# Kernel optimization log

Measured on AMD Instinct MI355X. Metric: run time of the kernel, lower is better.

Reference implementation:

```python
import jax, jax.numpy as jnp
import numpy as np

EPS = 1e-6  # clamp epsilon in GeM
NORM_EPS = 1e-12  # torch F.normalize eps
PATCH_SIZES = (3,)


def l2norm(x, axis):
    n = jnp.sqrt(jnp.sum(x * x, axis=axis, keepdims=True))
    return x / jnp.maximum(n, NORM_EPS)


def setup_inputs() -> dict:
    key = jax.random.key(0)
    k1, k2, k3 = jax.random.split(key, 3)
    N, D, H, W, F = 16, 2048, 32, 32, 512
    x = jax.random.normal(k1, (N, D, H, W), jnp.float32)
    proj_w = jax.random.normal(k2, (F, D), jnp.float32) * (1.0 / np.sqrt(D))
    proj_b = jax.random.normal(k3, (F,), jnp.float32) * 0.01
    p = jnp.full((1,), 3.0, jnp.float32)
    return {"x": x, "proj_w": proj_w, "proj_b": proj_b, "p": p}


def reference(x, proj_w, proj_b, p):
    # ---- GeM global descriptor (global_pool path inside local_pool) ----
    x = l2norm(x, axis=1)                                  # L2 over channel dim
    g = jnp.clip(x, EPS, None) ** p[0]                     # [N,D,H,W]
    g = g.mean(axis=(-2, -1))                              # [N,D]
    g = g ** (1.0 / p[0])
    g = g @ proj_w.T + proj_b                              # [N,F]
    g = l2norm(g, axis=1)

    # ---- integral image over spatial dims ----
    integ = jnp.cumsum(jnp.cumsum(x, axis=-1), axis=-2)    # [N,D,H,W]

    local_descs = []
    for ps in PATCH_SIZES:
        off = ps // 2
        # zero-pad (1+off) on top/left, then replicate-pad off on bottom/right
        ipad = jnp.pad(integ, ((0, 0), (0, 0), (1 + off, 0), (1 + off, 0)))
        ipad = jnp.pad(ipad, ((0, 0), (0, 0), (0, off), (0, off)), mode='edge')
        # box sum via 4-corner integral-image difference
        # == grouped 2x2 conv with dilation=ps, weights [[1,-1],[-1,1]], stride=1
        box = (ipad[:, :, :-ps, :-ps] - ipad[:, :, :-ps, ps:]
               - ipad[:, :, ps:, :-ps] + ipad[:, :, ps:, ps:])  # [N,D,H,W]
        N, D, Hh, Ww = box.shape
        pd = box.reshape(N, D, Hh * Ww).transpose(0, 2, 1)  # [N,HW,D]
        pd = pd @ proj_w.T + proj_b                         # [N,HW,F]
        pd = l2norm(pd, axis=2)
        local_descs.append(pd.transpose(0, 2, 1))           # [N,F,HW]

    return g, local_descs[0]
```

## Files before the change

### kernel.cpp

```cpp
#include <hip/hip_runtime.h>
#include <hip/hip_bf16.h>

#define N_ 16
#define D_ 2048
#define H_ 32
#define W_ 32
#define HW_ 1024
#define F_ 512

typedef unsigned short u16;
typedef unsigned int u32;
typedef __attribute__((ext_vector_type(8))) short bf16x8;
typedef __attribute__((ext_vector_type(4))) float f32x4;

__device__ __forceinline__ u16 f2bf(float f) {
  union { float fv; u32 u; } c; c.fv = f;
  u32 u = c.u;
  u32 r = (u + 0x7fffu + ((u >> 16) & 1u)) >> 16;
  return (u16)r;
}

#define GLD_LDS16(gp, lp) __builtin_amdgcn_global_load_lds( \
    (const __attribute__((address_space(1))) void*)(gp), \
    (__attribute__((address_space(3))) void*)(lp), 16, 0, 0)

__global__ __launch_bounds__(256) void k_zero(float* __restrict__ p) {
  int i = blockIdx.x * 256 + threadIdx.x;
  ((float4*)p)[i] = (float4){0.f, 0.f, 0.f, 0.f};
}

__global__ __launch_bounds__(256) void k_sumsq(const float* __restrict__ x, float* __restrict__ sumsq) {
  const int n = blockIdx.x;
  const int dc = blockIdx.y;
  const int t = threadIdx.x;
  const float* xp = x + ((size_t)n * D_ + (size_t)dc * 64) * HW_;
  float s0 = 0.f, s1 = 0.f, s2 = 0.f, s3 = 0.f;
  for (int d = 0; d < 64; ++d) {
    const float* row = xp + (size_t)d * HW_;
    float v0 = row[t], v1 = row[t + 256], v2 = row[t + 512], v3 = row[t + 768];
    s0 += v0 * v0; s1 += v1 * v1; s2 += v2 * v2; s3 += v3 * v3;
  }
  atomicAdd(&sumsq[n * HW_ + t      ], s0);
  atomicAdd(&sumsq[n * HW_ + t + 256], s1);
  atomicAdd(&sumsq[n * HW_ + t + 512], s2);
  atomicAdd(&sumsq[n * HW_ + t + 768], s3);
}

__global__ __launch_bounds__(256) void k_box2(const float* __restrict__ x,
    const float* __restrict__ sumsq, const float* __restrict__ pvec,
    float* __restrict__ gbuf, u16* __restrict__ packA) {
  const int n = blockIdx.x, ht = blockIdx.y, dc = blockIdx.z;
  const int h0 = ht * 4, d0 = dc * 64;
  const int t = threadIdx.x;
  const int w = t & 31, g = t >> 5;
  const float p = pvec[0];
  const bool p3 = (p == 3.0f);

  __shared__ __align__(16) u16 sbox[128 * 68];

  float rn[6];
  #pragma unroll
  for (int jj = 0; jj < 6; ++jj) {
    int hp = h0 - 1 + jj;
    float r = 0.f;
    if (hp >= 0 && hp < H_) r = 1.0f / fmaxf(sqrtf(sumsq[n * HW_ + hp * W_ + w]), 1e-12f);
    rn[jj] = r;
  }

  float s[8];
  #pragma unroll
  for (int j = 0; j < 8; ++j) s[j] = 0.f;

  #pragma unroll 2
  for (int j = 0; j < 8; ++j) {
    const int d = d0 + g * 8 + j;
    const float* col = x + ((size_t)(n * D_ + d)) * HW_ + w;
    float v[6];
    #pragma unroll
    for (int jj = 0; jj < 6; ++jj) {
      int hp = h0 - 1 + jj;
      float xv = (hp >= 0 && hp < H_) ? col[hp * W_] : 0.f;
      v[jj] = xv * rn[jj];
    }
    #pragma unroll
    for (int jj = 1; jj <= 4; ++jj) {
      float cv = fmaxf(v[jj], 1e-6f);
      s[j] += p3 ? cv * cv * cv : __powf(cv, p);
    }
    float hs[6];
    #pragma unroll
    for (int jj = 0; jj < 6; ++jj) {
      float l = __shfl_up(v[jj], 1, 32);
      float r = __shfl_down(v[jj], 1, 32);
      if (w == 0) l = 0.f;
      if (w == 31) r = 0.f;
      hs[jj] = l + v[jj] + r;
    }
    #pragma unroll
    for (int k = 0; k < 4; ++k) {
      float b = hs[k] + hs[k + 1] + hs[k + 2];
      sbox[(k * 32 + w) * 68 + g * 8 + j] = f2bf(b);
    }
  }
  __syncthreads();

  {
    const int r = t >> 1, half = t & 1;
    const u16* srcp = sbox + r * 68 + half * 32;
    uint2 a[8];
    #pragma unroll
    for (int q = 0; q < 8; ++q) a[q] = *(const uint2*)(srcp + q * 4);
    const int mt = n * 16 + ht * 2 + (r >> 6);
    const int mf = (r >> 4) & 3, r15 = r & 15;
    const int kt = dc * 2 + half;
    u16* dst = packA + ((size_t)(mt * 64 + kt) * 4 + mf) * 512 + r15 * 8;
    #pragma unroll
    for (int q = 0; q < 4; ++q) {
      uint4 b;
      b.x = a[2 * q].x; b.y = a[2 * q].y; b.z = a[2 * q + 1].x; b.w = a[2 * q + 1].y;
      *(uint4*)(dst + q * 128) = b;
    }
  }

  #pragma unroll
  for (int j = 0; j < 8; ++j) {
    float v = s[j];
    v += __shfl_xor(v, 16, 32);
    v += __shfl_xor(v, 8, 32);
    v += __shfl_xor(v, 4, 32);
    v += __shfl_xor(v, 2, 32);
    v += __shfl_xor(v, 1, 32);
    if (w == 0) atomicAdd(&gbuf[n * D_ + d0 + g * 8 + j], v);
  }
}

__global__ __launch_bounds__(256) void k_wconv(const float* __restrict__ w, u16* __restrict__ packB) {
  const int i = blockIdx.x * 256 + threadIdx.x;
  const int lane = i & 63, nf = (i >> 6) & 3, kt = (i >> 8) & 63, wq = i >> 14;
  const int r15 = lane & 15, hi = lane >> 4;
  const int f = wq * 64 + nf * 16 + r15;
  const int k = kt * 32 + hi * 8;
  const float* src = w + (size_t)f * D_ + k;
  float4 v0 = *(const float4*)(src);
  float4 v1 = *(const float4*)(src + 4);
  u16 r[8] = { f2bf(v0.x), f2bf(v0.y), f2bf(v0.z), f2bf(v0.w),
               f2bf(v1.x), f2bf(v1.y), f2bf(v1.z), f2bf(v1.w) };
  *(uint4*)(packB + (size_t)i * 8) = *(const uint4*)r;
}

__global__ __launch_bounds__(512) void k_gemm(const u16* __restrict__ packA,
    const u16* __restrict__ packB, const float* __restrict__ bias,
    float* __restrict__ outL) {
  const int n  = blockIdx.x >> 4;
  const int mtl = blockIdx.x & 15;
  const int mt = blockIdx.x;
  const int hw0 = mtl * 64;
  const int t = threadIdx.x;
  const int lane = t & 63, wv = t >> 6;
  const int r15 = lane & 15, hi = lane >> 4;

  __shared__ __align__(16) float smem_f[128 * 68];
  __shared__ float s_sq[8][64];
  __shared__ float s_rn[64];

  f32x4 acc[4][4];
  #pragma unroll
  for (int a = 0; a < 4; ++a)
    #pragma unroll
    for (int b = 0; b < 4; ++b) acc[a][b] = (f32x4){0.f, 0.f, 0.f, 0.f};

  const u16* asrc = packA + ((size_t)(mt * 64) * 4 + (wv & 3)) * 512 + lane * 8;
  const u16* bbase = packB + (size_t)wv * 131072 + lane * 8;

#define STAGE_A(KT) GLD_LDS16(asrc + (size_t)(KT) * 2048, \
    (char*)smem_f + ((KT) & 7) * 4096 + (wv & 3) * 1024)

  bf16x8 bc[4], bn[4];
  #pragma unroll
  for (int nf = 0; nf < 4; ++nf) bc[nf] = *(const bf16x8*)(bbase + nf * 512);
  __builtin_amdgcn_sched_barrier(0);
  #pragma unroll
  for (int q = 0; q < 5; ++q) STAGE_A(q);
  __builtin_amdgcn_sched_barrier(0);

  for (int kt = 0; kt < 64; ++kt) {
    if (kt + 1 < 64) {
      #pragma unroll
      for (int nf = 0; nf < 4; ++nf)
        bn[nf] = *(const bf16x8*)(bbase + ((kt + 1) * 4 + nf) * 512);
    }
    __builtin_amdgcn_sched_barrier(0);
    if (kt == 0) {
      asm volatile("s_waitcnt vmcnt(9)" ::: "memory");
    } else if (kt < 60) {
      asm volatile("s_waitcnt vmcnt(5)" ::: "memory");
    } else if (kt < 63) {
      asm volatile("s_waitcnt vmcnt(4)" ::: "memory");
    } else {
      asm volatile("s_waitcnt vmcnt(0)" ::: "memory");
    }
    __builtin_amdgcn_sched_barrier(0);
    __builtin_amdgcn_s_barrier();
    __builtin_amdgcn_sched_barrier(0);
    if (kt <= 58) STAGE_A(kt + 5);
    __builtin_amdgcn_sched_barrier(0);

    const u16* sA = (const u16*)((const char*)smem_f + (kt & 7) * 4096);
    bf16x8 af[4];
    #pragma unroll
    for (int mf = 0; mf < 4; ++mf)
      af[mf] = *(const bf16x8*)(sA + mf * 512 + lane * 8);
    #pragma unroll
    for (int mf = 0; mf < 4; ++mf)
      #pragma unroll
      for (int nf = 0; nf < 4; ++nf)
        acc[mf][nf] = __builtin_amdgcn_mfma_f32_16x16x32_bf16(af[mf], bc[nf], acc[mf][nf], 0, 0, 0);
    #pragma unroll
    for (int nf = 0; nf < 4; ++nf) bc[nf] = bn[nf];
  }
#undef STAGE_A

  float badd[4];
  #pragma unroll
  for (int nf = 0; nf < 4; ++nf) badd[nf] = bias[wv * 64 + nf * 16 + r15];
  #pragma unroll
  for (int mf = 0; mf < 4; ++mf)
    #pragma unroll
    for (int nf = 0; nf < 4; ++nf)
      #pragma unroll
      for (int j = 0; j < 4; ++j) acc[mf][nf][j] += badd[nf];

  #pragma unroll
  for (int mf = 0; mf < 4; ++mf)
    #pragma unroll
    for (int j = 0; j < 4; ++j) {
      float s = 0.f;
      #pragma unroll
      for (int nf = 0; nf < 4; ++nf) { float v = acc[mf][nf][j]; s += v * v; }
      s += __shfl_xor(s, 1); s += __shfl_xor(s, 2); s += __shfl_xor(s, 4); s += __shfl_xor(s, 8);
      if ((lane & 15) == 0) s_sq[wv][mf * 16 + hi * 4 + j] = s;
    }
  __syncthreads();
  if (t < 64) {
    float s = 0.f;
    #pragma unroll
    for (int w8 = 0; w8 < 8; ++w8) s += s_sq[w8][t];
    s_rn[t] = 1.0f / fmaxf(sqrtf(s), 1e-12f);
  }
  __syncthreads();

  float* ct = smem_f;
  for (int nf = 0; nf < 4; ++nf) {
    const int fi = wv * 16 + r15;
    #pragma unroll
    for (int mf = 0; mf < 4; ++mf)
      #pragma unroll
      for (int j = 0; j < 4; ++j) {
        int m = mf * 16 + hi * 4 + j;
        ct[fi * 68 + m] = acc[mf][nf][j] * s_rn[m];
      }
    __syncthreads();
    {
      int fr = t >> 2, mq = t & 3;
      int f = (fr >> 4) * 64 + nf * 16 + (fr & 15);
      float* dst = outL + ((size_t)(n * F_ + f)) * HW_ + hw0 + mq * 16;
      const float* srcp = ct + fr * 68 + mq * 16;
      float4 a0 = *(const float4*)(srcp);
      float4 a1 = *(const float4*)(srcp + 4);
      float4 a2 = *(const float4*)(srcp + 8);
      float4 a3 = *(const float4*)(srcp + 12);
      *(float4*)(dst) = a0; *(float4*)(dst + 4) = a1;
      *(float4*)(dst + 8) = a2; *(float4*)(dst + 12) = a3;
    }
    __syncthreads();
  }
}

__global__ __launch_bounds__(256) void k_gem_fin(const float* __restrict__ gbuf,
    const float* __restrict__ pvec, float* __restrict__ gg) {
  int i = blockIdx.x * 256 + threadIdx.x;
  float p = pvec[0];
  float m = gbuf[i] * (1.0f / 1024.0f);
  gg[i] = (p == 3.0f) ? cbrtf(m) : powf(m, 1.0f / p);
}

__global__ __launch_bounds__(256) void k_gproj(const float* __restrict__ w,
    const float* __restrict__ bias, const float* __restrict__ gg,
    float* __restrict__ gproj) {
  const int f = blockIdx.x;
  const int t = threadIdx.x;
  float wreg[8];
  #pragma unroll
  for (int j = 0; j < 8; ++j) wreg[j] = w[(size_t)f * D_ + t + j * 256];
  __shared__ float red[4];
  const int lane = t & 63, wv = t >> 6;
  for (int n = 0; n < N_; ++n) {
    float s = 0.f;
    #pragma unroll
    for (int j = 0; j < 8; ++j) s += wreg[j] * gg[n * D_ + t + j * 256];
    #pragma unroll
    for (int off = 32; off >= 1; off >>= 1) s += __shfl_down(s, off);
    if (lane == 0) red[wv] = s;
    __syncthreads();
    if (t == 0) gproj[n * F_ + f] = red[0] + red[1] + red[2] + red[3] + bias[f];
    __syncthreads();
  }
}

__global__ __launch_bounds__(512) void k_gnorm(const float* __restrict__ gproj, float* __restrict__ outg) {
  const int n = blockIdx.x;
  const int t = threadIdx.x;
  float v = gproj[n * F_ + t];
  float s = v * v;
  const int lane = t & 63, wv = t >> 6;
  #pragma unroll
  for (int off = 32; off >= 1; off >>= 1) s += __shfl_down(s, off);
  __shared__ float red[8];
  __shared__ float rtot;
  if (lane == 0) red[wv] = s;
  __syncthreads();
  if (t == 0) {
    float a = 0.f;
    #pragma unroll
    for (int i = 0; i < 8; ++i) a += red[i];
    rtot = 1.0f / fmaxf(sqrtf(a), 1e-12f);
  }
  __syncthreads();
  outg[n * F_ + t] = v * rtot;
}

extern "C" void kernel_launch(void* const* d_in, const int* in_sizes, int n_in,
                              void* d_out, int out_size, void* d_ws, size_t ws_size,
                              hipStream_t stream) {
  const float* x  = (const float*)d_in[0];
  const float* pw = (const float*)d_in[1];
  const float* pb = (const float*)d_in[2];
  const float* pv = (const float*)d_in[3];
  float* out = (float*)d_out;

  char* ws = (char*)d_ws;
  float* sumsq = (float*)ws;
  float* gbuf  = (float*)(ws + 65536);
  float* gg    = (float*)(ws + 65536 + 131072);
  float* gproj = (float*)(ws + 65536 + 2 * 131072);
  u16*   packB = (u16*)(ws + 65536 + 2 * 131072 + 32768);
  u16*   packA = (u16*)(ws + 4u * 1024u * 1024u);

  k_zero<<<dim3(48), dim3(256), 0, stream>>>(sumsq);
  k_sumsq<<<dim3(16, 32), dim3(256), 0, stream>>>(x, sumsq);
  k_wconv<<<dim3(512), dim3(256), 0, stream>>>(pw, packB);
  k_box2<<<dim3(16, 8, 32), dim3(256), 0, stream>>>(x, sumsq, pv, gbuf, packA);
  k_gem_fin<<<dim3(128), dim3(256), 0, stream>>>(gbuf, pv, gg);
  k_gproj<<<dim3(512), dim3(256), 0, stream>>>(pw, pb, gg, gproj);
  k_gnorm<<<dim3(16), dim3(512), 0, stream>>>(gproj, out);
  k_gemm<<<dim3(256), dim3(512), 0, stream>>>(packA, packB, pb, out + N_ * F_);
}
```

Baseline: 153.7 us.

## Stream box filter over rows per block and deepen B-prefetch in GEMM

```diff
diff --git a/kernel.cpp b/kernel.cpp
--- a/kernel.cpp
+++ b/kernel.cpp
@@ -49,8 +49,8 @@
 __global__ __launch_bounds__(256) void k_box2(const float* __restrict__ x,
     const float* __restrict__ sumsq, const float* __restrict__ pvec,
     float* __restrict__ gbuf, u16* __restrict__ packA) {
-  const int n = blockIdx.x, ht = blockIdx.y, dc = blockIdx.z;
-  const int h0 = ht * 4, d0 = dc * 64;
+  const int n = blockIdx.x, dc = blockIdx.y;
+  const int d0 = dc * 64;
   const int t = threadIdx.x;
   const int w = t & 31, g = t >> 5;
   const float p = pvec[0];
@@ -58,68 +58,77 @@
 
   __shared__ __align__(16) u16 sbox[128 * 68];
 
-  float rn[6];
-  #pragma unroll
-  for (int jj = 0; jj < 6; ++jj) {
-    int hp = h0 - 1 + jj;
-    float r = 0.f;
-    if (hp >= 0 && hp < H_) r = 1.0f / fmaxf(sqrtf(sumsq[n * HW_ + hp * W_ + w]), 1e-12f);
-    rn[jj] = r;
-  }
-
-  float s[8];
-  #pragma unroll
-  for (int j = 0; j < 8; ++j) s[j] = 0.f;
-
-  #pragma unroll 2
-  for (int j = 0; j < 8; ++j) {
-    const int d = d0 + g * 8 + j;
-    const float* col = x + ((size_t)(n * D_ + d)) * HW_ + w;
-    float v[6];
-    #pragma unroll
-    for (int jj = 0; jj < 6; ++jj) {
-      int hp = h0 - 1 + jj;
-      float xv = (hp >= 0 && hp < H_) ? col[hp * W_] : 0.f;
-      v[jj] = xv * rn[jj];
-    }
-    #pragma unroll
-    for (int jj = 1; jj <= 4; ++jj) {
-      float cv = fmaxf(v[jj], 1e-6f);
-      s[j] += p3 ? cv * cv * cv : __powf(cv, p);
-    }
-    float hs[6];
-    #pragma unroll
-    for (int jj = 0; jj < 6; ++jj) {
-      float l = __shfl_up(v[jj], 1, 32);
-      float r = __shfl_down(v[jj], 1, 32);
+  const float* xb = x + ((size_t)(n * D_ + d0 + g * 8)) * HW_ + w;
+  const float* sq = sumsq + n * HW_ + w;
+
+  float hc0[8], hc1[8], s[8];
+  {
+    float rn0 = 1.0f / fmaxf(sqrtf(sq[0]), 1e-12f);
+    #pragma unroll
+    for (int j = 0; j < 8; ++j) {
+      float v = xb[(size_t)j * HW_] * rn0;
+      float cv = fmaxf(v, 1e-6f);
+      s[j] = p3 ? cv * cv * cv : __powf(cv, p);
+      float l = __shfl_up(v, 1, 32), r = __shfl_down(v, 1, 32);
       if (w == 0) l = 0.f;
       if (w == 31) r = 0.f;
-      hs[jj] = l + v[jj] + r;
-    }
-    #pragma unroll
-    for (int k = 0; k < 4; ++k) {
-      float b = hs[k] + hs[k + 1] + hs[k + 2];
-      sbox[(k * 32 + w) * 68 + g * 8 + j] = f2bf(b);
-    }
-  }
-  __syncthreads();
-
-  {
-    const int r = t >> 1, half = t & 1;
-    const u16* srcp = sbox + r * 68 + half * 32;
-    uint2 a[8];
-    #pragma unroll
-    for (int q = 0; q < 8; ++q) a[q] = *(const uint2*)(srcp + q * 4);
-    const int mt = n * 16 + ht * 2 + (r >> 6);
-    const int mf = (r >> 4) & 3, r15 = r & 15;
-    const int kt = dc * 2 + half;
-    u16* dst = packA + ((size_t)(mt * 64 + kt) * 4 + mf) * 512 + r15 * 8;
+      hc0[j] = 0.f;
+      hc1[j] = l + v + r;
+    }
+  }
+
+  for (int ht = 0; ht < 8; ++ht) {
+    const int h0 = ht * 4;
+    float rnr[4];
     #pragma unroll
     for (int q = 0; q < 4; ++q) {
-      uint4 b;
-      b.x = a[2 * q].x; b.y = a[2 * q].y; b.z = a[2 * q + 1].x; b.w = a[2 * q + 1].y;
-      *(uint4*)(dst + q * 128) = b;
-    }
+      int hp = h0 + 1 + q;
+      rnr[q] = (hp < H_) ? 1.0f / fmaxf(sqrtf(sq[hp * W_]), 1e-12f) : 0.f;
+    }
+    #pragma unroll
+    for (int j = 0; j < 8; ++j) {
+      float hsq[4];
+      #pragma unroll
+      for (int q = 0; q < 4; ++q) {
+        int hp = h0 + 1 + q;
+        float v = 0.f;
+        if (hp < H_) {
+          v = xb[(size_t)j * HW_ + hp * W_] * rnr[q];
+          float cv = fmaxf(v, 1e-6f);
+          s[j] += p3 ? cv * cv * cv : __powf(cv, p);
+        }
+        float l = __shfl_up(v, 1, 32), r = __shfl_down(v, 1, 32);
+        if (w == 0) l = 0.f;
+        if (w == 31) r = 0.f;
+        hsq[q] = l + v + r;
+      }
+      u16* sb = sbox + (g * 8 + j);
+      sb[(0 * 32 + w) * 68] = f2bf(hc0[j] + hc1[j] + hsq[0]);
+      sb[(1 * 32 + w) * 68] = f2bf(hc1[j] + hsq[0] + hsq[1]);
+      sb[(2 * 32 + w) * 68] = f2bf(hsq[0] + hsq[1] + hsq[2]);
+      sb[(3 * 32 + w) * 68] = f2bf(hsq[1] + hsq[2] + hsq[3]);
+      hc0[j] = hsq[2];
+      hc1[j] = hsq[3];
+    }
+    __syncthreads();
+    {
+      const int r = t >> 1, half = t & 1;
+      const u16* srcp = sbox + r * 68 + half * 32;
+      uint2 a[8];
+      #pragma unroll
+      for (int q = 0; q < 8; ++q) a[q] = *(const uint2*)(srcp + q * 4);
+      const int mt = n * 16 + ht * 2 + (r >> 6);
+      const int mf = (r >> 4) & 3, r15 = r & 15;
+      const int kt = dc * 2 + half;
+      u16* dst = packA + ((size_t)(mt * 64 + kt) * 4 + mf) * 512 + r15 * 8;
+      #pragma unroll
+      for (int q = 0; q < 4; ++q) {
+        uint4 b;
+        b.x = a[2 * q].x; b.y = a[2 * q].y; b.z = a[2 * q + 1].x; b.w = a[2 * q + 1].y;
+        *(uint4*)(dst + q * 128) = b;
+      }
+    }
+    __syncthreads();
   }
 
   #pragma unroll
@@ -130,7 +139,7 @@
     v += __shfl_xor(v, 4, 32);
     v += __shfl_xor(v, 2, 32);
     v += __shfl_xor(v, 1, 32);
-    if (w == 0) atomicAdd(&gbuf[n * D_ + d0 + g * 8 + j], v);
+    if (w == 0) gbuf[n * D_ + d0 + g * 8 + j] = v;
   }
 }
 
@@ -175,26 +184,34 @@
 #define STAGE_A(KT) GLD_LDS16(asrc + (size_t)(KT) * 2048, \
     (char*)smem_f + ((KT) & 7) * 4096 + (wv & 3) * 1024)
 
-  bf16x8 bc[4], bn[4];
+  bf16x8 bc[4], bn[4], bn2[4];
   #pragma unroll
   for (int nf = 0; nf < 4; ++nf) bc[nf] = *(const bf16x8*)(bbase + nf * 512);
+  #pragma unroll
+  for (int nf = 0; nf < 4; ++nf) bn[nf] = *(const bf16x8*)(bbase + (4 + nf) * 512);
   __builtin_amdgcn_sched_barrier(0);
   #pragma unroll
   for (int q = 0; q < 5; ++q) STAGE_A(q);
   __builtin_amdgcn_sched_barrier(0);
 
   for (int kt = 0; kt < 64; ++kt) {
-    if (kt + 1 < 64) {
+    if (kt + 2 < 64) {
       #pragma unroll
       for (int nf = 0; nf < 4; ++nf)
-        bn[nf] = *(const bf16x8*)(bbase + ((kt + 1) * 4 + nf) * 512);
+        bn2[nf] = *(const bf16x8*)(bbase + ((kt + 2) * 4 + nf) * 512);
     }
     __builtin_amdgcn_sched_barrier(0);
     if (kt == 0) {
+      asm volatile("s_waitcnt vmcnt(8)" ::: "memory");
+    } else if (kt == 1) {
+      asm volatile("s_waitcnt vmcnt(12)" ::: "memory");
+    } else if (kt < 60) {
+      asm volatile("s_waitcnt vmcnt(10)" ::: "memory");
+    } else if (kt == 60) {
       asm volatile("s_waitcnt vmcnt(9)" ::: "memory");
-    } else if (kt < 60) {
-      asm volatile("s_waitcnt vmcnt(5)" ::: "memory");
-    } else if (kt < 63) {
+    } else if (kt == 61) {
+      asm volatile("s_waitcnt vmcnt(8)" ::: "memory");
+    } else if (kt == 62) {
       asm volatile("s_waitcnt vmcnt(4)" ::: "memory");
     } else {
       asm volatile("s_waitcnt vmcnt(0)" ::: "memory");
@@ -216,7 +233,7 @@
       for (int nf = 0; nf < 4; ++nf)
         acc[mf][nf] = __builtin_amdgcn_mfma_f32_16x16x32_bf16(af[mf], bc[nf], acc[mf][nf], 0, 0, 0);
     #pragma unroll
-    for (int nf = 0; nf < 4; ++nf) bc[nf] = bn[nf];
+    for (int nf = 0; nf < 4; ++nf) { bc[nf] = bn[nf]; bn[nf] = bn2[nf]; }
   }
 #undef STAGE_A
 
@@ -346,10 +363,10 @@
   u16*   packB = (u16*)(ws + 65536 + 2 * 131072 + 32768);
   u16*   packA = (u16*)(ws + 4u * 1024u * 1024u);
 
-  k_zero<<<dim3(48), dim3(256), 0, stream>>>(sumsq);
+  k_zero<<<dim3(16), dim3(256), 0, stream>>>(sumsq);
   k_sumsq<<<dim3(16, 32), dim3(256), 0, stream>>>(x, sumsq);
   k_wconv<<<dim3(512), dim3(256), 0, stream>>>(pw, packB);
-  k_box2<<<dim3(16, 8, 32), dim3(256), 0, stream>>>(x, sumsq, pv, gbuf, packA);
+  k_box2<<<dim3(16, 32), dim3(256), 0, stream>>>(x, sumsq, pv, gbuf, packA);
   k_gem_fin<<<dim3(128), dim3(256), 0, stream>>>(gbuf, pv, gg);
   k_gproj<<<dim3(512), dim3(256), 0, stream>>>(pw, pb, gg, gproj);
   k_gnorm<<<dim3(16), dim3(512), 0, stream>>>(gproj, out);
```

Result: slower. 199.7 us (+29.9%).
